# Kernel tuning notes

Hardware: AMD Instinct MI355X
Metric: run time of the kernel (lower is better)

Reference implementation:

```python
import jax, jax.numpy as jnp
import numpy as np

REG_PARAM = 0.0002
COS_EPS = 1e-8  # torch F.cosine_similarity eps


def setup_inputs() -> dict:
    key = jax.random.key(0)
    k1, k2, k3, k4 = jax.random.split(key, 4)
    return {
        "output": jax.random.normal(k1, (32, 3, 256, 256), dtype=jnp.float32),
        "ground_truth": jax.random.normal(k2, (32, 3, 256, 256), dtype=jnp.float32),
        "att": jax.random.normal(k3, (8192, 2000), dtype=jnp.float32),
        "mem": jax.random.normal(k4, (2000, 256), dtype=jnp.float32),
    }


def reference(output, ground_truth, att, mem):
    # MSE reconstruction loss (mean reduction)
    mse = jnp.mean((ground_truth - output) ** 2)

    # Entropy regularizer: sum(softmax * log_softmax) over att, dim=1
    logp = jax.nn.log_softmax(att, axis=1)
    reg = jnp.sum(jnp.exp(logp) * logp)
    loss = mse - REG_PARAM * reg

    # Pairwise cosine-similarity sum over memory vectors:
    # original: nested loop over all i<j pairs; here: normalize + Gram + triu sum
    norms = jnp.maximum(jnp.linalg.norm(mem, axis=1, keepdims=True), COS_EPS)
    unit = mem / norms                      # [N, D]
    gram = unit @ unit.T                    # [N, N]
    cos_sum = jnp.sum(jnp.triu(gram, k=1))  # strict upper triangle = i<j pairs

    return loss + cos_sum
```

## Files before the change

kernel.cpp:

```cpp
#include <hip/hip_runtime.h>
#include <math.h>

#define REG_PARAM 0.0002f
#define COS_EPS 1e-8f

#define MAIN_BLOCKS 2048
#define MEM_BLOCKS 32
#define TOTAL_BLOCKS (MAIN_BLOCKS + MEM_BLOCKS)

#define WS_MSE  0
#define WS_ENT  2048
#define WS_DIAG 4096
#define WS_COL  4352

__device__ __forceinline__ float waveReduceSum(float v) {
    #pragma unroll
    for (int off = 32; off > 0; off >>= 1)
        v += __shfl_xor(v, off, 64);
    return v;
}

__device__ __forceinline__ float blockReduceSum(float v, float* sh) {
    v = waveReduceSum(v);
    int wid = threadIdx.x >> 6, lane = threadIdx.x & 63;
    __syncthreads();
    if (lane == 0) sh[wid] = v;
    __syncthreads();
    return sh[0] + sh[1] + sh[2] + sh[3];
}

__global__ void partials_kernel(const float4* __restrict__ out4,
                                const float4* __restrict__ gt4,
                                const float4* __restrict__ att4,
                                const float4* __restrict__ mem4,
                                float* __restrict__ ws, int n4) {
    __shared__ float sh[4 * 256];
    __shared__ float shd[4];
    const int b = blockIdx.x;
    const int t = threadIdx.x;
    const int wid = t >> 6, lane = t & 63;

    if (b < MAIN_BLOCKS) {
        float acc = 0.f;
        for (int i = b * 256 + t; i < n4; i += MAIN_BLOCKS * 256) {
            float4 a = out4[i], g = gt4[i];
            float d0 = g.x - a.x, d1 = g.y - a.y;
            float d2 = g.z - a.z, d3 = g.w - a.w;
            acc += d0 * d0 + d1 * d1 + d2 * d2 + d3 * d3;
        }
        acc = waveReduceSum(acc);
        if (lane == 0) sh[wid] = acc;

        const int row = b * 4 + wid;
        const float4* __restrict__ rp = att4 + (size_t)row * 500;
        float z = 0.f, tt = 0.f;
        #pragma unroll
        for (int k = 0; k < 8; ++k) {
            int idx = lane + (k << 6);
            if (idx < 500) {
                float4 x = rp[idx];
                float e;
                e = __expf(x.x); z += e; tt += x.x * e;
                e = __expf(x.y); z += e; tt += x.y * e;
                e = __expf(x.z); z += e; tt += x.z * e;
                e = __expf(x.w); z += e; tt += x.w * e;
            }
        }
        z = waveReduceSum(z);
        tt = waveReduceSum(tt);
        float ent = tt / z - __logf(z);
        if (lane == 1) sh[4 + wid] = ent;
        __syncthreads();
        if (t == 0) {
            ws[WS_MSE + b] = sh[0] + sh[1] + sh[2] + sh[3];
            ws[WS_ENT + b] = sh[4] + sh[5] + sh[6] + sh[7];
        }
    } else {
        const int mb = b - MAIN_BLOCKS;
        const int wglobal = mb * 4 + wid;
        float c0 = 0.f, c1 = 0.f, c2 = 0.f, c3 = 0.f, dacc = 0.f;
        for (int row = wglobal; row < 2000; row += MEM_BLOCKS * 4) {
            float4 v = mem4[(size_t)row * 64 + lane];
            float ss = v.x * v.x + v.y * v.y + v.z * v.z + v.w * v.w;
            ss = waveReduceSum(ss);
            float inv = 1.f / fmaxf(sqrtf(ss), COS_EPS);
            c0 += v.x * inv; c1 += v.y * inv; c2 += v.z * inv; c3 += v.w * inv;
            if (lane == 0) dacc += ss * inv * inv;
        }
        if (lane == 0) shd[wid] = dacc;
        sh[wid * 256 + lane * 4 + 0] = c0;
        sh[wid * 256 + lane * 4 + 1] = c1;
        sh[wid * 256 + lane * 4 + 2] = c2;
        sh[wid * 256 + lane * 4 + 3] = c3;
        __syncthreads();
        ws[WS_COL + mb * 256 + t] = sh[t] + sh[256 + t] + sh[512 + t] + sh[768 + t];
        if (t == 0) ws[WS_DIAG + mb] = shd[0] + shd[1] + shd[2] + shd[3];
    }
}

__global__ void finalize_kernel(const float* __restrict__ ws,
                                float* __restrict__ out, float inv_n) {
    __shared__ float sh[4];
    const int t = threadIdx.x;

    float v = 0.f;
    #pragma unroll
    for (int k = 0; k < 8; ++k) v += ws[WS_MSE + t + (k << 8)];
    float msesum = blockReduceSum(v, sh);

    v = 0.f;
    #pragma unroll
    for (int k = 0; k < 8; ++k) v += ws[WS_ENT + t + (k << 8)];
    float entsum = blockReduceSum(v, sh);

    float S = 0.f;
    #pragma unroll
    for (int mb = 0; mb < 32; ++mb) S += ws[WS_COL + (mb << 8) + t];
    float ssum = blockReduceSum(S * S, sh);

    float dv = (t < 32) ? ws[WS_DIAG + t] : 0.f;
    float diag = blockReduceSum(dv, sh);

    if (t == 0) {
        out[0] = msesum * inv_n - REG_PARAM * entsum + 0.5f * (ssum - diag);
    }
}

extern "C" void kernel_launch(void* const* d_in, const int* in_sizes, int n_in,
                              void* d_out, int out_size, void* d_ws, size_t ws_size,
                              hipStream_t stream) {
    const float* out_img = (const float*)d_in[0];
    const float* gt      = (const float*)d_in[1];
    const float* att     = (const float*)d_in[2];
    const float* mem     = (const float*)d_in[3];
    float* ws = (float*)d_ws;
    float* out = (float*)d_out;

    int n = in_sizes[0];
    int n4 = n / 4;

    partials_kernel<<<TOTAL_BLOCKS, 256, 0, stream>>>(
        (const float4*)out_img, (const float4*)gt,
        (const float4*)att, (const float4*)mem, ws, n4);
    finalize_kernel<<<1, 256, 0, stream>>>(ws, out, 1.0f / (float)n);
}
```

Measured before the change: 32.27 us.

## Halve main blocks, batch all loads per thread, hardcode sizes, pre-scale partials

Main blocks go from 2048 to 1024. Each thread now issues six MSE float4 load pairs and eight att float4 loads per row up front, with loops fully unrolled for more memory-level parallelism, and each wave handles two att rows. The MSE size and scale are hardcoded as compile-time constants, and each block writes one combined, pre-scaled partial, which shrinks the finalize reduction. The kernel no longer checks input size, so it only works for the fixed shape, and MEM blocks move to the front of the grid.

Result: faster. 29.56 us (-8.4%).

```diff
diff --git a/kernel.cpp b/kernel.cpp
--- a/kernel.cpp
+++ b/kernel.cpp
@@ -3,15 +3,16 @@
 
 #define REG_PARAM 0.0002f
 #define COS_EPS 1e-8f
+#define INV_N (1.0f / 6291456.0f)
 
-#define MAIN_BLOCKS 2048
 #define MEM_BLOCKS 32
-#define TOTAL_BLOCKS (MAIN_BLOCKS + MEM_BLOCKS)
+#define MAIN_BLOCKS 1024
+#define TOTAL_BLOCKS (MEM_BLOCKS + MAIN_BLOCKS)
+#define MSE_STRIDE 262144
 
-#define WS_MSE  0
-#define WS_ENT  2048
-#define WS_DIAG 4096
-#define WS_COL  4352
+#define WS_MAIN 0
+#define WS_DIAG 1024
+#define WS_COL  1280
 
 __device__ __forceinline__ float waveReduceSum(float v) {
     #pragma unroll
@@ -33,50 +34,98 @@
                                 const float4* __restrict__ gt4,
                                 const float4* __restrict__ att4,
                                 const float4* __restrict__ mem4,
-                                float* __restrict__ ws, int n4) {
+                                float* __restrict__ ws) {
     __shared__ float sh[4 * 256];
     __shared__ float shd[4];
-    const int b = blockIdx.x;
     const int t = threadIdx.x;
     const int wid = t >> 6, lane = t & 63;
 
-    if (b < MAIN_BLOCKS) {
-        float acc = 0.f;
-        for (int i = b * 256 + t; i < n4; i += MAIN_BLOCKS * 256) {
-            float4 a = out4[i], g = gt4[i];
-            float d0 = g.x - a.x, d1 = g.y - a.y;
-            float d2 = g.z - a.z, d3 = g.w - a.w;
-            acc += d0 * d0 + d1 * d1 + d2 * d2 + d3 * d3;
+    if (blockIdx.x >= MEM_BLOCKS) {
+        const int b = blockIdx.x - MEM_BLOCKS;
+        const int base = (b << 8) + t;
+        float mse_acc = 0.f;
+        float ent_acc = 0.f;
+        #pragma unroll
+        for (int c = 0; c < 2; ++c) {
+            float4 a0 = out4[base + (c * 3 + 0) * MSE_STRIDE];
+            float4 g0 = gt4 [base + (c * 3 + 0) * MSE_STRIDE];
+            float4 a1 = out4[base + (c * 3 + 1) * MSE_STRIDE];
+            float4 g1 = gt4 [base + (c * 3 + 1) * MSE_STRIDE];
+            float4 a2 = out4[base + (c * 3 + 2) * MSE_STRIDE];
+            float4 g2 = gt4 [base + (c * 3 + 2) * MSE_STRIDE];
+            const int row = (((b << 2) + wid) << 1) + c;
+            const float4* __restrict__ rp = att4 + (size_t)row * 500;
+            float4 x0 = rp[lane];
+            float4 x1 = rp[lane + 64];
+            float4 x2 = rp[lane + 128];
+            float4 x3 = rp[lane + 192];
+            float4 x4 = rp[lane + 256];
+            float4 x5 = rp[lane + 320];
+            float4 x6 = rp[lane + 384];
+            float4 x7 = rp[(lane + 448 < 500) ? (lane + 448) : 499];
+
+            float d;
+            d = g0.x - a0.x; mse_acc += d * d;
+            d = g0.y - a0.y; mse_acc += d * d;
+            d = g0.z - a0.z; mse_acc += d * d;
+            d = g0.w - a0.w; mse_acc += d * d;
+            d = g1.x - a1.x; mse_acc += d * d;
+            d = g1.y - a1.y; mse_acc += d * d;
+            d = g1.z - a1.z; mse_acc += d * d;
+            d = g1.w - a1.w; mse_acc += d * d;
+            d = g2.x - a2.x; mse_acc += d * d;
+            d = g2.y - a2.y; mse_acc += d * d;
+            d = g2.z - a2.z; mse_acc += d * d;
+            d = g2.w - a2.w; mse_acc += d * d;
+
+            float z = 0.f, tt = 0.f, e;
+            e = __expf(x0.x); z += e; tt += x0.x * e;
+            e = __expf(x0.y); z += e; tt += x0.y * e;
+            e = __expf(x0.z); z += e; tt += x0.z * e;
+            e = __expf(x0.w); z += e; tt += x0.w * e;
+            e = __expf(x1.x); z += e; tt += x1.x * e;
+            e = __expf(x1.y); z += e; tt += x1.y * e;
+            e = __expf(x1.z); z += e; tt += x1.z * e;
+            e = __expf(x1.w); z += e; tt += x1.w * e;
+            e = __expf(x2.x); z += e; tt += x2.x * e;
+            e = __expf(x2.y); z += e; tt += x2.y * e;
+            e = __expf(x2.z); z += e; tt += x2.z * e;
+            e = __expf(x2.w); z += e; tt += x2.w * e;
+            e = __expf(x3.x); z += e; tt += x3.x * e;
+            e = __expf(x3.y); z += e; tt += x3.y * e;
+            e = __expf(x3.z); z += e; tt += x3.z * e;
+            e = __expf(x3.w); z += e; tt += x3.w * e;
+            e = __expf(x4.x); z += e; tt += x4.x * e;
+            e = __expf(x4.y); z += e; tt += x4.y * e;
+            e = __expf(x4.z); z += e; tt += x4.z * e;
+            e = __expf(x4.w); z += e; tt += x4.w * e;
+            e = __expf(x5.x); z += e; tt += x5.x * e;
+            e = __expf(x5.y); z += e; tt += x5.y * e;
+            e = __expf(x5.z); z += e; tt += x5.z * e;
+            e = __expf(x5.w); z += e; tt += x5.w * e;
+            e = __expf(x6.x); z += e; tt += x6.x * e;
+            e = __expf(x6.y); z += e; tt += x6.y * e;
+            e = __expf(x6.z); z += e; tt += x6.z * e;
+            e = __expf(x6.w); z += e; tt += x6.w * e;
+            if (lane + 448 < 500) {
+                e = __expf(x7.x); z += e; tt += x7.x * e;
+                e = __expf(x7.y); z += e; tt += x7.y * e;
+                e = __expf(x7.z); z += e; tt += x7.z * e;
+                e = __expf(x7.w); z += e; tt += x7.w * e;
+            }
+            z = waveReduceSum(z);
+            tt = waveReduceSum(tt);
+            ent_acc += tt / z - __logf(z);
         }
-        acc = waveReduceSum(acc);
-        if (lane == 0) sh[wid] = acc;
-
-        const int row = b * 4 + wid;
-        const float4* __restrict__ rp = att4 + (size_t)row * 500;
-        float z = 0.f, tt = 0.f;
-        #pragma unroll
-        for (int k = 0; k < 8; ++k) {
-            int idx = lane + (k << 6);
-            if (idx < 500) {
-                float4 x = rp[idx];
-                float e;
-                e = __expf(x.x); z += e; tt += x.x * e;
-                e = __expf(x.y); z += e; tt += x.y * e;
-                e = __expf(x.z); z += e; tt += x.z * e;
-                e = __expf(x.w); z += e; tt += x.w * e;
-            }
-        }
-        z = waveReduceSum(z);
-        tt = waveReduceSum(tt);
-        float ent = tt / z - __logf(z);
-        if (lane == 1) sh[4 + wid] = ent;
+        mse_acc = waveReduceSum(mse_acc);
+        if (lane == 0) { sh[wid] = mse_acc; sh[4 + wid] = ent_acc; }
         __syncthreads();
         if (t == 0) {
-            ws[WS_MSE + b] = sh[0] + sh[1] + sh[2] + sh[3];
-            ws[WS_ENT + b] = sh[4] + sh[5] + sh[6] + sh[7];
+            ws[WS_MAIN + b] = (sh[0] + sh[1] + sh[2] + sh[3]) * INV_N
+                            - REG_PARAM * (sh[4] + sh[5] + sh[6] + sh[7]);
         }
     } else {
-        const int mb = b - MAIN_BLOCKS;
+        const int mb = blockIdx.x;
         const int wglobal = mb * 4 + wid;
         float c0 = 0.f, c1 = 0.f, c2 = 0.f, c3 = 0.f, dacc = 0.f;
         for (int row = wglobal; row < 2000; row += MEM_BLOCKS * 4) {
@@ -98,20 +147,14 @@
     }
 }
 
-__global__ void finalize_kernel(const float* __restrict__ ws,
-                                float* __restrict__ out, float inv_n) {
+__global__ void finalize_kernel(const float* __restrict__ ws, float* __restrict__ out) {
     __shared__ float sh[4];
     const int t = threadIdx.x;
 
     float v = 0.f;
     #pragma unroll
-    for (int k = 0; k < 8; ++k) v += ws[WS_MSE + t + (k << 8)];
-    float msesum = blockReduceSum(v, sh);
-
-    v = 0.f;
-    #pragma unroll
-    for (int k = 0; k < 8; ++k) v += ws[WS_ENT + t + (k << 8)];
-    float entsum = blockReduceSum(v, sh);
+    for (int k = 0; k < 4; ++k) v += ws[WS_MAIN + t + (k << 8)];
+    float mainsum = blockReduceSum(v, sh);
 
     float S = 0.f;
     #pragma unroll
@@ -122,7 +165,7 @@
     float diag = blockReduceSum(dv, sh);
 
     if (t == 0) {
-        out[0] = msesum * inv_n - REG_PARAM * entsum + 0.5f * (ssum - diag);
+        out[0] = mainsum + 0.5f * (ssum - diag);
     }
 }
 
@@ -136,11 +179,8 @@
     float* ws = (float*)d_ws;
     float* out = (float*)d_out;
 
-    int n = in_sizes[0];
-    int n4 = n / 4;
-
     partials_kernel<<<TOTAL_BLOCKS, 256, 0, stream>>>(
         (const float4*)out_img, (const float4*)gt,
-        (const float4*)att, (const float4*)mem, ws, n4);
-    finalize_kernel<<<1, 256, 0, stream>>>(ws, out, 1.0f / (float)n);
+        (const float4*)att, (const float4*)mem, ws);
+    finalize_kernel<<<1, 256, 0, stream>>>(ws, out);
 }
```
